# Optimization experiments

Measured on AMD Instinct MI355X. Metric: run time of the kernel, lower is better.

The kernel has to match this reference:

```python
import jax, jax.numpy as jnp
import numpy as np

S, L, E = 64, 256, 768          # sentences, tokens per sentence, BERT hidden
N, P = 4096, 32768              # events, event pairs
C, H, D = 256, 4, 64            # CGE channels, heads, head dim (C = H*D = n_last)
M = 8                           # max event span length
MLP_H = 1024
ITERS = 3                       # max_iteration + 1
RATE = 0.5
BETA_INTRA, BETA_INTER = 0.5, 0.5


def setup_inputs():
    key = jax.random.key(0)
    ks = jax.random.split(key, 16)
    nrm = lambda k, shape, sc: jax.random.normal(k, shape, dtype=jnp.float32) * sc
    event_start = jax.random.randint(ks[2], (N,), 0, L - M)
    span = jax.random.randint(ks[3], (N,), 1, M + 1)
    return {
        "sent_emb": nrm(ks[0], (S, L, E), 1.0),
        "proj_in_W": nrm(ks[7], (E, C), E ** -0.5),
        "proj_in_b": jnp.zeros((C,), jnp.float32),
        "proj_W": nrm(ks[8], (C, C), C ** -0.5),
        "proj_b": jnp.zeros((C,), jnp.float32),
        "att_src_intra": nrm(ks[9], (H, D), D ** -0.5),
        "att_dst_intra": nrm(ks[10], (H, D), D ** -0.5),
        "att_src_inter": nrm(ks[11], (H, D), D ** -0.5),
        "att_dst_inter": nrm(ks[12], (H, D), D ** -0.5),
        "mlp_W1": nrm(ks[13], (C + 2 * E, MLP_H), (C + 2 * E) ** -0.5),
        "mlp_b1": jnp.zeros((MLP_H,), jnp.float32),
        "mlp_W2": nrm(ks[14], (MLP_H, 3), MLP_H ** -0.5),
        "mlp_b2": jnp.zeros((3,), jnp.float32),
        "event_sent": jax.random.randint(ks[1], (N,), 0, S),
        "event_start": event_start,
        "event_end": event_start + span,
        "pair_idx": jax.random.randint(ks[4], (P, 2), 0, N),
        "rel_type": jax.random.randint(ks[5], (P,), 0, 2),
        "target": jax.random.randint(ks[6], (P,), 0, 3),
    }


def _attend(h, src, dst, emask, att_src, att_dst):
    # h: [N,H,D]. Masked graph attention, softmax over incoming edges per dst.
    a = jax.nn.leaky_relu((h[src] * att_src).sum(-1) + (h[dst] * att_dst).sum(-1), 0.2)  # [En,H]
    a = jnp.where(emask[:, None], a, -1e9)
    amax = jnp.maximum(jax.ops.segment_max(a, dst, num_segments=N), -1e9)  # [N,H]
    ex = jnp.exp(a - amax[dst]) * emask[:, None].astype(a.dtype)
    denom = jax.ops.segment_sum(ex, dst, num_segments=N)
    alpha = ex / (denom[dst] + 1e-9)
    out = jax.ops.segment_sum(alpha[:, :, None] * h[src], dst, num_segments=N)  # [N,H,D]
    return out.reshape(N, H * D)


def _forward(sent_emb, proj_in_W, proj_in_b, proj_W, proj_b,
             att_src_intra, att_dst_intra, att_src_inter, att_dst_inter,
             mlp_W1, mlp_b1, mlp_W2, mlp_b2,
             event_sent, event_start, event_end, pair_idx, rel_type, target):
    # extract_event: mean of sentence token embeddings over each event span
    pos = event_start[:, None] + jnp.arange(M)                      # [N,M]
    vmask = (pos < event_end[:, None]).astype(sent_emb.dtype)       # [N,M]
    tok = sent_emb[event_sent[:, None], jnp.clip(pos, 0, L - 1)]    # [N,M,E]
    e_emb = (tok * vmask[..., None]).sum(1) / (event_end - event_start).astype(sent_emb.dtype)[:, None]

    p0, p1 = pair_idx[:, 0], pair_idx[:, 1]
    pair_emb = jnp.concatenate([e_emb[p0], e_emb[p1]], axis=-1)     # [P,2E]
    x = e_emb @ proj_in_W + proj_in_b                               # [N,C]

    self_idx = jnp.arange(N)
    ones_n = jnp.ones((N,), bool)
    src_all = jnp.concatenate([p0, p1])
    dst_all = jnp.concatenate([p1, p0])
    intra2 = jnp.concatenate([rel_type == 0, rel_type == 0])

    loss = jnp.float32(0.0)
    pred = None
    for it in range(ITERS):
        diff = x[p0] - x[p1]                                        # [P,C]
        pre = jnp.concatenate([pair_emb, diff], axis=-1)            # [P,2E+C]
        pred = jax.nn.relu(pre @ mlp_W1 + mlp_b1) @ mlp_W2 + mlp_b2  # [P,3]
        logp = jax.nn.log_softmax(pred, axis=-1)
        loss = loss + (1.0 / (it + 1)) * (-jnp.take_along_axis(logp, target[:, None], axis=1).mean())

        # data-dependent edge construction (masked, fixed-size edge lists)
        psoft = jax.nn.softmax(pred, axis=-1)
        conf = psoft.max(1) > RATE
        parg = psoft.argmax(1)
        m_all = jnp.concatenate([conf & (parg == 1), conf & (parg == 2)])

        h = (x @ proj_W + proj_b).reshape(N, H, D)
        # intra edges + always-on self loops
        src_i = jnp.concatenate([src_all, self_idx])
        dst_i = jnp.concatenate([dst_all, self_idx])
        m_i = jnp.concatenate([m_all & intra2, ones_n])
        out_intra = _attend(h, src_i, dst_i, m_i, att_src_intra, att_dst_intra)
        out_inter = _attend(h, src_all, dst_all, m_all & (~intra2), att_src_inter, att_dst_inter)
        x = BETA_INTRA * out_intra + BETA_INTER * out_inter
    return loss, pred


def reference(sent_emb, proj_in_W, proj_in_b, proj_W, proj_b,
              att_src_intra, att_dst_intra, att_src_inter, att_dst_inter,
              mlp_W1, mlp_b1, mlp_W2, mlp_b2,
              event_sent, event_start, event_end, pair_idx, rel_type, target):
    return _forward(sent_emb, proj_in_W, proj_in_b, proj_W, proj_b,
                    att_src_intra, att_dst_intra, att_src_inter, att_dst_inter,
                    mlp_W1, mlp_b1, mlp_W2, mlp_b2,
                    event_sent, event_start, event_end, pair_idx, rel_type, target)
```

## Files before the change

### kernel.cpp

```cpp
#include <hip/hip_runtime.h>
#include <cstddef>
#include <cstdint>

#define NEV   4096
#define NPAIR 32768
#define NEDGE (2*NPAIR)
#define EDIM  768
#define CDIM  256
#define MLPH  1024
#define LLEN  256

typedef unsigned short u16;
typedef __attribute__((ext_vector_type(8))) short bhalf8;
typedef __attribute__((ext_vector_type(4))) float f32x4;

#define GLOAD_LDS(g, l) __builtin_amdgcn_global_load_lds( \
    (const __attribute__((address_space(1))) unsigned int*)(g), \
    (__attribute__((address_space(3))) unsigned int*)(l), 16, 0, 0)

__device__ inline u16 f2bf(float f) {
  union { float f; unsigned u; } v; v.f = f;
  unsigned r = v.u + 0x7fffu + ((v.u >> 16) & 1u);
  return (u16)(r >> 16);
}
__device__ inline float bf2f(u16 h) {
  union { unsigned u; float f; } v; v.u = ((unsigned)h) << 16; return v.f;
}

__global__ void k_zero(int* __restrict__ deg, int* __restrict__ pdeg,
                       float* __restrict__ out) {
  int i = blockIdx.x * 256 + threadIdx.x;
  if (i < NEV) { deg[i] = 0; pdeg[i] = 0; }
  if (i == 0) out[0] = 0.f;
}

__global__ void k_embed(const float* __restrict__ sent, const int* __restrict__ es,
                        const int* __restrict__ st, const int* __restrict__ en,
                        u16* __restrict__ Ahat) {
  int node = blockIdx.x;
  int s = es[node];
  int a = st[node];
  int span = en[node] - a;
  float fspan = (float)span;
  const float* base = sent + ((size_t)s * LLEN + a) * EDIM;
  for (int d = threadIdx.x; d < EDIM; d += 256) {
    float acc = 0.f;
    for (int m = 0; m < span; ++m) acc += base[(size_t)m * EDIM + d];
    float e = acc / fspan;
    u16 hi = f2bf(e);
    float lo = e - bf2f(hi);
    size_t b = (size_t)node * (2 * EDIM);
    Ahat[b + d] = hi;
    Ahat[b + EDIM + d] = f2bf(lo);
  }
}

__global__ void k_countF(const int* __restrict__ pair, int* __restrict__ deg,
                         int* __restrict__ pdeg) {
  int e = blockIdx.x * 256 + threadIdx.x;
  if (e >= NEDGE) return;
  int p = (e < NPAIR) ? e : e - NPAIR;
  int dst = (e < NPAIR) ? pair[2 * p + 1] : pair[2 * p];
  atomicAdd(&deg[dst], 1);
  if (e < NPAIR) atomicAdd(&pdeg[pair[2 * e]], 1);
}

__device__ inline void scan_body(const int* __restrict__ deg, int* __restrict__ rowp,
                                 int* __restrict__ cursor, int* part) {
  int t = threadIdx.x;
  int base = t * 16;
  int sum = 0;
  for (int i = 0; i < 16; ++i) sum += deg[base + i];
  part[t] = sum;
  __syncthreads();
  for (int off = 1; off < 256; off <<= 1) {
    int v = (t >= off) ? part[t - off] : 0;
    __syncthreads();
    part[t] += v;
    __syncthreads();
  }
  int run = (t == 0) ? 0 : part[t - 1];
  for (int i = 0; i < 16; ++i) {
    rowp[base + i] = run;
    cursor[base + i] = 0;
    run += deg[base + i];
  }
  if (t == 255) rowp[NEV] = run;
}

__global__ void k_scanF(const int* __restrict__ deg, int* __restrict__ rowp,
                        int* __restrict__ cursor, const int* __restrict__ pdeg,
                        int* __restrict__ prow, int* __restrict__ pcur) {
  __shared__ int part[256];
  scan_body(deg, rowp, cursor, part);
  __syncthreads();
  scan_body(pdeg, prow, pcur, part);
}

__global__ void k_scatterF(const int* __restrict__ pair, const int* __restrict__ rowp,
                           int* __restrict__ cursor, int* __restrict__ e_src,
                           int* __restrict__ e_id, const int* __restrict__ prow,
                           int* __restrict__ pcur, int* __restrict__ pidx) {
  int e = blockIdx.x * 256 + threadIdx.x;
  if (e >= NEDGE) return;
  int p   = (e < NPAIR) ? e : e - NPAIR;
  int src = (e < NPAIR) ? pair[2 * p]     : pair[2 * p + 1];
  int dst = (e < NPAIR) ? pair[2 * p + 1] : pair[2 * p];
  int pos = rowp[dst] + atomicAdd(&cursor[dst], 1);
  e_src[pos] = src;
  e_id[pos]  = e;
  if (e < NPAIR) {
    int pp = prow[pair[2 * e]] + atomicAdd(&pcur[pair[2 * e]], 1);
    pidx[pp] = e;
  }
}

__global__ __launch_bounds__(256) void cvt_w(const float* __restrict__ W1,
                                             const float* __restrict__ piW,
                                             const float* __restrict__ projW,
                                             u16* __restrict__ BTe,
                                             u16* __restrict__ BTu)
{
  __shared__ float tile[32][33];
  int which = (blockIdx.y >= 24) ? 1 : 0;
  if (which && blockIdx.x >= 40) return;
  u16* BT = which ? BTu : BTe;
  int K = which ? CDIM : EDIM;
  int ld = K * 2;
  int bk = (which ? (blockIdx.y - 24) : blockIdx.y) * 32;
  int bc = blockIdx.x * 32;
  int tx = threadIdx.x & 31, ty = threadIdx.x >> 5;
#pragma unroll
  for (int rr = 0; rr < 4; ++rr) {
    int k = bk + ty + rr * 8;
    int c = bc + tx;
    float v;
    if (which == 0) {
      v = (c < 1024) ? W1[(size_t)k * MLPH + c]
        : (c < 2048) ? W1[(size_t)(EDIM + k) * MLPH + (c - 1024)]
        : piW[(size_t)k * CDIM + (c - 2048)];
    } else {
      v = (c < 1024) ? W1[(size_t)(2 * EDIM + k) * MLPH + c]
        : projW[(size_t)k * CDIM + (c - 1024)];
    }
    tile[ty + rr * 8][tx] = v;
  }
  __syncthreads();
#pragma unroll
  for (int rr = 0; rr < 4; ++rr) {
    int c = bc + ty + rr * 8;
    int k = bk + tx;
    float v = tile[tx][ty + rr * 8];
    u16 hi = f2bf(v);
    float lo = v - bf2f(hi);
    size_t b = (size_t)c * ld;
    BT[b + k] = hi;
    BT[b + K + k] = f2bf(lo);
  }
}

__global__ __launch_bounds__(256) void mgemm(
    const u16* __restrict__ A, const u16* __restrict__ BT, int K, int mode,
    float* __restrict__ G1, float* __restrict__ G2, u16* __restrict__ Xhat,
    const float* __restrict__ pib, const float* __restrict__ b1,
    const float* __restrict__ pb, float* __restrict__ U, float* __restrict__ V,
    float* __restrict__ h, const float* __restrict__ asi,
    const float* __restrict__ adi, const float* __restrict__ asj,
    const float* __restrict__ adj, float* __restrict__ sv)
{
  __shared__ u16 Ash[64 * 32];
  __shared__ u16 Asl[64 * 32];
  __shared__ u16 Bsh[128 * 32];
  __shared__ u16 Bsl[128 * 32];
  int tid = threadIdx.x;
  int wave = tid >> 6, lane = tid & 63;
  int bm = blockIdx.y * 64, bn = blockIdx.x * 128;
  int wm = (wave >> 1) * 32, wn = (wave & 1) * 64;

  int Kp2 = 2 * K;
  int srow = tid >> 2;
  int scol = (tid & 3) << 3;
  const u16* AgH = A + (size_t)(bm + srow) * Kp2 + scol;
  const u16* BgH = BT + (size_t)(bn + srow) * Kp2 + scol;
  const u16* BgH2 = BT + (size_t)(bn + 64 + srow) * Kp2 + scol;

  f32x4 acc[2][4];
#pragma unroll
  for (int i = 0; i < 2; ++i)
#pragma unroll
    for (int j = 0; j < 4; ++j) {
      f32x4 z = {0.f, 0.f, 0.f, 0.f};
      acc[i][j] = z;
    }

  int fr = lane & 15;
  int fq = lane >> 4;

  for (int kc = 0; kc < K; kc += 32) {
    GLOAD_LDS(AgH + kc,       &Ash[tid * 8]);
    GLOAD_LDS(AgH + K + kc,   &Asl[tid * 8]);
    GLOAD_LDS(BgH + kc,       &Bsh[tid * 8]);
    GLOAD_LDS(BgH2 + kc,      &Bsh[2048 + tid * 8]);
    GLOAD_LDS(BgH + K + kc,   &Bsl[tid * 8]);
    GLOAD_LDS(BgH2 + K + kc,  &Bsl[2048 + tid * 8]);
    __syncthreads();
    bhalf8 afh[2], afl[2], bfh[4], bfl[4];
#pragma unroll
    for (int i = 0; i < 2; ++i) {
      afh[i] = *(const bhalf8*)&Ash[(wm + i * 16 + fr) * 32 + fq * 8];
      afl[i] = *(const bhalf8*)&Asl[(wm + i * 16 + fr) * 32 + fq * 8];
    }
#pragma unroll
    for (int j = 0; j < 4; ++j) {
      bfh[j] = *(const bhalf8*)&Bsh[(wn + j * 16 + fr) * 32 + fq * 8];
      bfl[j] = *(const bhalf8*)&Bsl[(wn + j * 16 + fr) * 32 + fq * 8];
    }
#pragma unroll
    for (int i = 0; i < 2; ++i)
#pragma unroll
      for (int j = 0; j < 4; ++j) {
        acc[i][j] = __builtin_amdgcn_mfma_f32_16x16x32_bf16(afh[i], bfh[j], acc[i][j], 0, 0, 0);
        acc[i][j] = __builtin_amdgcn_mfma_f32_16x16x32_bf16(afh[i], bfl[j], acc[i][j], 0, 0, 0);
        acc[i][j] = __builtin_amdgcn_mfma_f32_16x16x32_bf16(afl[i], bfh[j], acc[i][j], 0, 0, 0);
      }
    __syncthreads();
  }

#pragma unroll
  for (int i = 0; i < 2; ++i) {
    int mrow = bm + wm + i * 16 + fq * 4;
#pragma unroll
    for (int g = 0; g < 4; ++g) {
      int m = mrow + g;
#pragma unroll
      for (int j = 0; j < 4; ++j) {
        int c = bn + wn + j * 16 + fr;
        float vv = acc[i][j][g];
        if (mode == 0) {
          if (c < 1024) {
            G1[(size_t)m * MLPH + c] = vv;
          } else if (c < 2048) {
            G2[(size_t)m * MLPH + (c - 1024)] = vv;
          } else {
            int cc = c - 2048;
            float xv = vv + pib[cc];
            u16 hi = f2bf(xv);
            float lo = xv - bf2f(hi);
            size_t b = (size_t)m * (2 * CDIM);
            Xhat[b + cc] = hi;
            Xhat[b + CDIM + cc] = f2bf(lo);
          }
        } else {
          if (c < 1024) {
            size_t idx = (size_t)m * MLPH + c;
            U[idx] = G1[idx] + vv + b1[c];
            V[idx] = G2[idx] - vv;
          } else {
            int cc = c - 1024;
            h[(size_t)m * CDIM + cc] = vv + pb[cc];
          }
        }
      }
    }
  }

  if (mode == 1 && bn >= MLPH) {
    int hbase = bn - MLPH + wn;
    int head = hbase >> 6;
#pragma unroll
    for (int i = 0; i < 2; ++i) {
#pragma unroll
      for (int g = 0; g < 4; ++g) {
        int m = bm + wm + i * 16 + fq * 4 + g;
        float p0 = 0.f, p1 = 0.f, p2 = 0.f, p3 = 0.f;
#pragma unroll
        for (int j = 0; j < 4; ++j) {
          int hc = hbase + j * 16 + fr;
          float hv = acc[i][j][g] + pb[hc];
          p0 += hv * asi[hc];
          p1 += hv * adi[hc];
          p2 += hv * asj[hc];
          p3 += hv * adj[hc];
        }
#pragma unroll
        for (int mm = 1; mm < 16; mm <<= 1) {
          p0 += __shfl_xor(p0, mm);
          p1 += __shfl_xor(p1, mm);
          p2 += __shfl_xor(p2, mm);
          p3 += __shfl_xor(p3, mm);
        }
        if (fr == 0) {
          sv[0 * NEV * 4 + m * 4 + head] = p0;
          sv[1 * NEV * 4 + m * 4 + head] = p1;
          sv[2 * NEV * 4 + m * 4 + head] = p2;
          sv[3 * NEV * 4 + m * 4 + head] = p3;
        }
      }
    }
  }
}

__global__ __launch_bounds__(256) void k_pred_g(
    const float* __restrict__ U, const float* __restrict__ V,
    const int* __restrict__ pair, const int* __restrict__ prow,
    const int* __restrict__ pidx, const float* __restrict__ W2,
    const float* __restrict__ b2, const int* __restrict__ target,
    int* __restrict__ mstate, float* __restrict__ out,
    float* __restrict__ partials, float lossCoef)
{
  __shared__ float ush[MLPH];
  __shared__ float red[4];
  int n = blockIdx.x;
  int tid = threadIdx.x;
  const float* u = U + (size_t)n * MLPH;
#pragma unroll
  for (int i = 0; i < 4; ++i) ush[tid + i * 256] = u[tid + i * 256];
  __syncthreads();
  int wv = tid >> 6, lane = tid & 63;
  int beg = prow[n], end = prow[n + 1];
  float lsum = 0.f;
  for (int ip = beg + wv; ip < end; ip += 4) {
    int p = pidx[ip];
    int i1 = pair[2 * p + 1];
    const float* v = V + (size_t)i1 * MLPH;
    float a0 = 0.f, a1 = 0.f, a2 = 0.f;
    for (int kb = (lane << 2); kb < MLPH; kb += 256) {
      float4 uu = *(const float4*)(&ush[kb]);
      float4 vv = *(const float4*)(v + kb);
      float h0 = fmaxf(uu.x + vv.x, 0.f);
      float h1 = fmaxf(uu.y + vv.y, 0.f);
      float h2 = fmaxf(uu.z + vv.z, 0.f);
      float h3 = fmaxf(uu.w + vv.w, 0.f);
      const float4* w4 = (const float4*)(W2 + 3 * kb);
      float4 wa = w4[0], wb = w4[1], wc = w4[2];
      a0 += h0 * wa.x + h1 * wa.w + h2 * wb.z + h3 * wc.y;
      a1 += h0 * wa.y + h1 * wb.x + h2 * wb.w + h3 * wc.z;
      a2 += h0 * wa.z + h1 * wb.y + h2 * wc.x + h3 * wc.w;
    }
#pragma unroll
    for (int m = 32; m >= 1; m >>= 1) {
      a0 += __shfl_down(a0, m);
      a1 += __shfl_down(a1, m);
      a2 += __shfl_down(a2, m);
    }
    if (lane == 0) {
      a0 += b2[0]; a1 += b2[1]; a2 += b2[2];
      float mx = fmaxf(a0, fmaxf(a1, a2));
      float e0 = expf(a0 - mx), e1 = expf(a1 - mx), e2 = expf(a2 - mx);
      float sum = e0 + e1 + e2;
      int arg = 0; float best = e0;
      if (e1 > best) { best = e1; arg = 1; }
      if (e2 > best) { best = e2; arg = 2; }
      bool conf = (best / sum) > 0.5f;
      mstate[p] = conf ? arg : -1;
      int t = target[p];
      float predt = (t == 0) ? a0 : ((t == 1) ? a1 : a2);
      float logp = (predt - mx) - logf(sum);
      lsum += -logp * lossCoef;
      float* po = out + 1 + (size_t)p * 3;
      po[0] = a0; po[1] = a1; po[2] = a2;
    }
  }
  if (lane == 0) red[wv] = lsum;
  __syncthreads();
  if (tid == 0) partials[n] = red[0] + red[1] + red[2] + red[3];
}

__global__ __launch_bounds__(256) void k_attn(
    const float* __restrict__ h, const float* __restrict__ sv,
    const int* __restrict__ rowp, const int* __restrict__ e_src,
    const int* __restrict__ e_id, const int* __restrict__ mstate,
    const int* __restrict__ rel, u16* __restrict__ Xhat,
    const float* __restrict__ lpart, float* __restrict__ out)
{
  int node = blockIdx.x;
  int t = threadIdx.x;
  int head = t >> 6;
  const float* s_si = sv;
  const float* s_di = sv + NEV * 4;
  const float* s_sj = sv + 2 * NEV * 4;
  const float* s_dj = sv + 3 * NEV * 4;
  float sdi = s_di[node * 4 + head];
  float sdj = s_dj[node * 4 + head];
  int beg = rowp[node], end = rowp[node + 1];
  float aself = s_si[node * 4 + head] + sdi;
  aself = aself > 0.f ? aself : 0.2f * aself;
  float mxi = aself;
  float mxj = -1e9f;
  for (int e = beg; e < end; ++e) {
    int eid = e_id[e];
    int pp = (eid < NPAIR) ? eid : eid - NPAIR;
    int st = mstate[pp];
    bool mall = (eid < NPAIR) ? (st == 1) : (st == 2);
    if (!mall) continue;
    int src = e_src[e];
    if (rel[pp] == 0) {
      float a = s_si[src * 4 + head] + sdi;
      a = a > 0.f ? a : 0.2f * a;
      mxi = fmaxf(mxi, a);
    } else {
      float a = s_sj[src * 4 + head] + sdj;
      a = a > 0.f ? a : 0.2f * a;
      mxj = fmaxf(mxj, a);
    }
  }
  float deni = 0.f, denj = 0.f, acci = 0.f, accj = 0.f;
  {
    float ex = expf(aself - mxi);
    deni += ex;
    acci += ex * h[(size_t)node * CDIM + t];
  }
  for (int e = beg; e < end; ++e) {
    int eid = e_id[e];
    int pp = (eid < NPAIR) ? eid : eid - NPAIR;
    int st = mstate[pp];
    bool mall = (eid < NPAIR) ? (st == 1) : (st == 2);
    if (!mall) continue;
    int src = e_src[e];
    float hval = h[(size_t)src * CDIM + t];
    if (rel[pp] == 0) {
      float a = s_si[src * 4 + head] + sdi;
      a = a > 0.f ? a : 0.2f * a;
      float ex = expf(a - mxi);
      deni += ex; acci += ex * hval;
    } else {
      float a = s_sj[src * 4 + head] + sdj;
      a = a > 0.f ? a : 0.2f * a;
      float ex = expf(a - mxj);
      denj += ex; accj += ex * hval;
    }
  }
  float outv = 0.5f * (acci / (deni + 1e-9f)) + 0.5f * (accj / (denj + 1e-9f));
  u16 hi = f2bf(outv);
  float lo = outv - bf2f(hi);
  size_t b = (size_t)node * (2 * CDIM);
  Xhat[b + t] = hi;
  Xhat[b + CDIM + t] = f2bf(lo);

  if (blockIdx.x == 0) {
    __shared__ float sm[256];
    float s = 0.f;
    for (int i = t; i < NEV; i += 256) s += lpart[i];
    sm[t] = s;
    __syncthreads();
    for (int off = 128; off; off >>= 1) {
      if (t < off) sm[t] += sm[t + off];
      __syncthreads();
    }
    if (t == 0) out[0] += sm[0];
  }
}

extern "C" void kernel_launch(void* const* d_in, const int* in_sizes, int n_in,
                              void* d_out, int out_size, void* d_ws, size_t ws_size,
                              hipStream_t stream)
{
  const float* sent      = (const float*)d_in[0];
  const float* proj_in_W = (const float*)d_in[1];
  const float* proj_in_b = (const float*)d_in[2];
  const float* proj_W    = (const float*)d_in[3];
  const float* proj_b    = (const float*)d_in[4];
  const float* asi       = (const float*)d_in[5];
  const float* adi       = (const float*)d_in[6];
  const float* asj       = (const float*)d_in[7];
  const float* adj       = (const float*)d_in[8];
  const float* W1        = (const float*)d_in[9];
  const float* b1        = (const float*)d_in[10];
  const float* W2        = (const float*)d_in[11];
  const float* b2        = (const float*)d_in[12];
  const int*   es        = (const int*)d_in[13];
  const int*   st        = (const int*)d_in[14];
  const int*   en        = (const int*)d_in[15];
  const int*   pair      = (const int*)d_in[16];
  const int*   rel       = (const int*)d_in[17];
  const int*   target    = (const int*)d_in[18];
  float* out = (float*)d_out;

  char* w = (char*)d_ws;
  auto alloc = [&](size_t bytes) -> char* {
    char* p = w;
    w += (bytes + 255) & ~(size_t)255;
    return p;
  };
  u16*   Ahat = (u16*)alloc(sizeof(u16) * (size_t)NEV * 2 * EDIM);
  u16*   BTe  = (u16*)alloc(sizeof(u16) * (size_t)2304 * 1536);
  u16*   BTu  = (u16*)alloc(sizeof(u16) * (size_t)1280 * 512);
  u16*   Xhat = (u16*)alloc(sizeof(u16) * (size_t)NEV * 2 * CDIM);
  float* G1   = (float*)alloc(sizeof(float) * (size_t)NEV * MLPH);
  float* G2   = (float*)alloc(sizeof(float) * (size_t)NEV * MLPH);
  float* U    = (float*)alloc(sizeof(float) * (size_t)NEV * MLPH);
  float* V    = (float*)alloc(sizeof(float) * (size_t)NEV * MLPH);
  float* h    = (float*)alloc(sizeof(float) * (size_t)NEV * CDIM);
  float* sv   = (float*)alloc(sizeof(float) * (size_t)NEV * 16);
  float* lpart= (float*)alloc(sizeof(float) * NEV);
  int* deg    = (int*)alloc(sizeof(int) * NEV);
  int* rowp   = (int*)alloc(sizeof(int) * (NEV + 1));
  int* cursor = (int*)alloc(sizeof(int) * NEV);
  int* e_src  = (int*)alloc(sizeof(int) * NEDGE);
  int* e_id   = (int*)alloc(sizeof(int) * NEDGE);
  int* pdeg   = (int*)alloc(sizeof(int) * NEV);
  int* prow   = (int*)alloc(sizeof(int) * (NEV + 1));
  int* pcur   = (int*)alloc(sizeof(int) * NEV);
  int* pidx   = (int*)alloc(sizeof(int) * NPAIR);
  int* mstate = (int*)alloc(sizeof(int) * NPAIR);

  k_zero<<<(NEV + 255) / 256, 256, 0, stream>>>(deg, pdeg, out);
  k_embed<<<NEV, 256, 0, stream>>>(sent, es, st, en, Ahat);
  k_countF<<<NEDGE / 256, 256, 0, stream>>>(pair, deg, pdeg);
  k_scanF<<<1, 256, 0, stream>>>(deg, rowp, cursor, pdeg, prow, pcur);
  k_scatterF<<<NEDGE / 256, 256, 0, stream>>>(pair, rowp, cursor, e_src, e_id,
                                              prow, pcur, pidx);
  cvt_w<<<dim3(72, 32), 256, 0, stream>>>(W1, proj_in_W, proj_W, BTe, BTu);

  mgemm<<<dim3(2304 / 128, NEV / 64), 256, 0, stream>>>(
      Ahat, BTe, EDIM, 0, G1, G2, Xhat, proj_in_b,
      nullptr, nullptr, nullptr, nullptr, nullptr,
      nullptr, nullptr, nullptr, nullptr, nullptr);

  for (int it = 0; it < 3; ++it) {
    mgemm<<<dim3(1280 / 128, NEV / 64), 256, 0, stream>>>(
        Xhat, BTu, CDIM, 1, G1, G2, nullptr, nullptr,
        b1, proj_b, U, V, h, asi, adi, asj, adj, sv);
    float coef = 1.0f / ((float)(it + 1) * (float)NPAIR);
    k_pred_g<<<NEV, 256, 0, stream>>>(U, V, pair, prow, pidx, W2, b2, target,
                                      mstate, out, lpart, coef);
    k_attn<<<NEV, 256, 0, stream>>>(h, sv, rowp, e_src, e_id, mstate, rel, Xhat,
                                    lpart, out);
  }
  (void)in_sizes; (void)n_in; (void)out_size; (void)ws_size;
}
```

Before: 503.8 us.

## Double-buffer GEMM LDS staging and merge prep kernels into one launch

```diff
diff --git a/kernel.cpp b/kernel.cpp
--- a/kernel.cpp
+++ b/kernel.cpp
@@ -27,32 +27,86 @@
   union { unsigned u; float f; } v; v.u = ((unsigned)h) << 16; return v.f;
 }
 
-__global__ void k_zero(int* __restrict__ deg, int* __restrict__ pdeg,
-                       float* __restrict__ out) {
-  int i = blockIdx.x * 256 + threadIdx.x;
+__global__ __launch_bounds__(256) void k_prep(
+    const float* __restrict__ sent, const int* __restrict__ es,
+    const int* __restrict__ st, const int* __restrict__ en,
+    u16* __restrict__ Ahat, const float* __restrict__ W1,
+    const float* __restrict__ piW, const float* __restrict__ projW,
+    u16* __restrict__ BTe, u16* __restrict__ BTu,
+    int* __restrict__ deg, int* __restrict__ pdeg, float* __restrict__ out)
+{
+  __shared__ float tile[32][33];
+  int b = blockIdx.x;
+  int tid = threadIdx.x;
+  if (b < NEV) {
+    int node = b;
+    int s = es[node];
+    int a = st[node];
+    int span = en[node] - a;
+    float fspan = (float)span;
+    const float* base = sent + ((size_t)s * LLEN + a) * EDIM;
+    if (tid < 192) {
+      int d0 = tid * 4;
+      float4 acc = {0.f, 0.f, 0.f, 0.f};
+      for (int m = 0; m < span; ++m) {
+        float4 v = *(const float4*)(base + (size_t)m * EDIM + d0);
+        acc.x += v.x; acc.y += v.y; acc.z += v.z; acc.w += v.w;
+      }
+      float e[4] = {acc.x / fspan, acc.y / fspan, acc.z / fspan, acc.w / fspan};
+      ushort4 hiv, lov;
+      u16 h0 = f2bf(e[0]); lov.x = f2bf(e[0] - bf2f(h0)); hiv.x = h0;
+      u16 h1 = f2bf(e[1]); lov.y = f2bf(e[1] - bf2f(h1)); hiv.y = h1;
+      u16 h2 = f2bf(e[2]); lov.z = f2bf(e[2] - bf2f(h2)); hiv.z = h2;
+      u16 h3 = f2bf(e[3]); lov.w = f2bf(e[3] - bf2f(h3)); hiv.w = h3;
+      size_t bo = (size_t)node * (2 * EDIM);
+      *(ushort4*)&Ahat[bo + d0] = hiv;
+      *(ushort4*)&Ahat[bo + EDIM + d0] = lov;
+    }
+    return;
+  }
+  if (b < NEV + 2304) {
+    int id = b - NEV;
+    int bxx = id % 72, byy = id / 72;
+    int which = (byy >= 24) ? 1 : 0;
+    if (which && bxx >= 40) return;
+    u16* BT = which ? BTu : BTe;
+    int K = which ? CDIM : EDIM;
+    int ld = K * 2;
+    int bk = (which ? (byy - 24) : byy) * 32;
+    int bc = bxx * 32;
+    int tx = tid & 31, ty = tid >> 5;
+#pragma unroll
+    for (int rr = 0; rr < 4; ++rr) {
+      int k = bk + ty + rr * 8;
+      int c = bc + tx;
+      float v;
+      if (which == 0) {
+        v = (c < 1024) ? W1[(size_t)k * MLPH + c]
+          : (c < 2048) ? W1[(size_t)(EDIM + k) * MLPH + (c - 1024)]
+          : piW[(size_t)k * CDIM + (c - 2048)];
+      } else {
+        v = (c < 1024) ? W1[(size_t)(2 * EDIM + k) * MLPH + c]
+          : projW[(size_t)k * CDIM + (c - 1024)];
+      }
+      tile[ty + rr * 8][tx] = v;
+    }
+    __syncthreads();
+#pragma unroll
+    for (int rr = 0; rr < 4; ++rr) {
+      int c = bc + ty + rr * 8;
+      int k = bk + tx;
+      float v = tile[tx][ty + rr * 8];
+      u16 hi = f2bf(v);
+      float lo = v - bf2f(hi);
+      size_t bb = (size_t)c * ld;
+      BT[bb + k] = hi;
+      BT[bb + K + k] = f2bf(lo);
+    }
+    return;
+  }
+  int i = (b - NEV - 2304) * 256 + tid;
   if (i < NEV) { deg[i] = 0; pdeg[i] = 0; }
   if (i == 0) out[0] = 0.f;
-}
-
-__global__ void k_embed(const float* __restrict__ sent, const int* __restrict__ es,
-                        const int* __restrict__ st, const int* __restrict__ en,
-                        u16* __restrict__ Ahat) {
-  int node = blockIdx.x;
-  int s = es[node];
-  int a = st[node];
-  int span = en[node] - a;
-  float fspan = (float)span;
-  const float* base = sent + ((size_t)s * LLEN + a) * EDIM;
-  for (int d = threadIdx.x; d < EDIM; d += 256) {
-    float acc = 0.f;
-    for (int m = 0; m < span; ++m) acc += base[(size_t)m * EDIM + d];
-    float e = acc / fspan;
-    u16 hi = f2bf(e);
-    float lo = e - bf2f(hi);
-    size_t b = (size_t)node * (2 * EDIM);
-    Ahat[b + d] = hi;
-    Ahat[b + EDIM + d] = f2bf(lo);
-  }
 }
 
 __global__ void k_countF(const int* __restrict__ pair, int* __restrict__ deg,
@@ -115,50 +169,6 @@
   }
 }
 
-__global__ __launch_bounds__(256) void cvt_w(const float* __restrict__ W1,
-                                             const float* __restrict__ piW,
-                                             const float* __restrict__ projW,
-                                             u16* __restrict__ BTe,
-                                             u16* __restrict__ BTu)
-{
-  __shared__ float tile[32][33];
-  int which = (blockIdx.y >= 24) ? 1 : 0;
-  if (which && blockIdx.x >= 40) return;
-  u16* BT = which ? BTu : BTe;
-  int K = which ? CDIM : EDIM;
-  int ld = K * 2;
-  int bk = (which ? (blockIdx.y - 24) : blockIdx.y) * 32;
-  int bc = blockIdx.x * 32;
-  int tx = threadIdx.x & 31, ty = threadIdx.x >> 5;
-#pragma unroll
-  for (int rr = 0; rr < 4; ++rr) {
-    int k = bk + ty + rr * 8;
-    int c = bc + tx;
-    float v;
-    if (which == 0) {
-      v = (c < 1024) ? W1[(size_t)k * MLPH + c]
-        : (c < 2048) ? W1[(size_t)(EDIM + k) * MLPH + (c - 1024)]
-        : piW[(size_t)k * CDIM + (c - 2048)];
-    } else {
-      v = (c < 1024) ? W1[(size_t)(2 * EDIM + k) * MLPH + c]
-        : projW[(size_t)k * CDIM + (c - 1024)];
-    }
-    tile[ty + rr * 8][tx] = v;
-  }
-  __syncthreads();
-#pragma unroll
-  for (int rr = 0; rr < 4; ++rr) {
-    int c = bc + ty + rr * 8;
-    int k = bk + tx;
-    float v = tile[tx][ty + rr * 8];
-    u16 hi = f2bf(v);
-    float lo = v - bf2f(hi);
-    size_t b = (size_t)c * ld;
-    BT[b + k] = hi;
-    BT[b + K + k] = f2bf(lo);
-  }
-}
-
 __global__ __launch_bounds__(256) void mgemm(
     const u16* __restrict__ A, const u16* __restrict__ BT, int K, int mode,
     float* __restrict__ G1, float* __restrict__ G2, u16* __restrict__ Xhat,
@@ -168,10 +178,10 @@
     const float* __restrict__ adi, const float* __restrict__ asj,
     const float* __restrict__ adj, float* __restrict__ sv)
 {
-  __shared__ u16 Ash[64 * 32];
-  __shared__ u16 Asl[64 * 32];
-  __shared__ u16 Bsh[128 * 32];
-  __shared__ u16 Bsl[128 * 32];
+  __shared__ u16 Ash[2 * 64 * 32];
+  __shared__ u16 Asl[2 * 64 * 32];
+  __shared__ u16 Bsh[2 * 128 * 32];
+  __shared__ u16 Bsl[2 * 128 * 32];
   int tid = threadIdx.x;
   int wave = tid >> 6, lane = tid & 63;
   int bm = blockIdx.y * 64, bn = blockIdx.x * 128;
@@ -180,9 +190,22 @@
   int Kp2 = 2 * K;
   int srow = tid >> 2;
   int scol = (tid & 3) << 3;
-  const u16* AgH = A + (size_t)(bm + srow) * Kp2 + scol;
-  const u16* BgH = BT + (size_t)(bn + srow) * Kp2 + scol;
+  const u16* AgH  = A + (size_t)(bm + srow) * Kp2 + scol;
+  const u16* BgH  = BT + (size_t)(bn + srow) * Kp2 + scol;
   const u16* BgH2 = BT + (size_t)(bn + 64 + srow) * Kp2 + scol;
+
+  auto STAGE = [&](int buf, int kc) {
+    u16* as = Ash + buf * 2048;
+    u16* al = Asl + buf * 2048;
+    u16* bs = Bsh + buf * 4096;
+    u16* bl = Bsl + buf * 4096;
+    GLOAD_LDS(AgH + kc,       &as[tid * 8]);
+    GLOAD_LDS(AgH + K + kc,   &al[tid * 8]);
+    GLOAD_LDS(BgH + kc,       &bs[tid * 8]);
+    GLOAD_LDS(BgH2 + kc,      &bs[2048 + tid * 8]);
+    GLOAD_LDS(BgH + K + kc,   &bl[tid * 8]);
+    GLOAD_LDS(BgH2 + K + kc,  &bl[2048 + tid * 8]);
+  };
 
   f32x4 acc[2][4];
 #pragma unroll
@@ -196,24 +219,25 @@
   int fr = lane & 15;
   int fq = lane >> 4;
 
+  STAGE(0, 0);
+  __syncthreads();
+  int cur = 0;
   for (int kc = 0; kc < K; kc += 32) {
-    GLOAD_LDS(AgH + kc,       &Ash[tid * 8]);
-    GLOAD_LDS(AgH + K + kc,   &Asl[tid * 8]);
-    GLOAD_LDS(BgH + kc,       &Bsh[tid * 8]);
-    GLOAD_LDS(BgH2 + kc,      &Bsh[2048 + tid * 8]);
-    GLOAD_LDS(BgH + K + kc,   &Bsl[tid * 8]);
-    GLOAD_LDS(BgH2 + K + kc,  &Bsl[2048 + tid * 8]);
-    __syncthreads();
+    if (kc + 32 < K) STAGE(cur ^ 1, kc + 32);
+    const u16* as = Ash + cur * 2048;
+    const u16* al = Asl + cur * 2048;
+    const u16* bs = Bsh + cur * 4096;
+    const u16* bl = Bsl + cur * 4096;
     bhalf8 afh[2], afl[2], bfh[4], bfl[4];
 #pragma unroll
     for (int i = 0; i < 2; ++i) {
-      afh[i] = *(const bhalf8*)&Ash[(wm + i * 16 + fr) * 32 + fq * 8];
-      afl[i] = *(const bhalf8*)&Asl[(wm + i * 16 + fr) * 32 + fq * 8];
+      afh[i] = *(const bhalf8*)&as[(wm + i * 16 + fr) * 32 + fq * 8];
+      afl[i] = *(const bhalf8*)&al[(wm + i * 16 + fr) * 32 + fq * 8];
     }
 #pragma unroll
     for (int j = 0; j < 4; ++j) {
-      bfh[j] = *(const bhalf8*)&Bsh[(wn + j * 16 + fr) * 32 + fq * 8];
-      bfl[j] = *(const bhalf8*)&Bsl[(wn + j * 16 + fr) * 32 + fq * 8];
+      bfh[j] = *(const bhalf8*)&bs[(wn + j * 16 + fr) * 32 + fq * 8];
+      bfl[j] = *(const bhalf8*)&bl[(wn + j * 16 + fr) * 32 + fq * 8];
     }
 #pragma unroll
     for (int i = 0; i < 2; ++i)
@@ -224,6 +248,7 @@
         acc[i][j] = __builtin_amdgcn_mfma_f32_16x16x32_bf16(afl[i], bfh[j], acc[i][j], 0, 0, 0);
       }
     __syncthreads();
+    cur ^= 1;
   }
 
 #pragma unroll
@@ -504,13 +529,13 @@
   int* pidx   = (int*)alloc(sizeof(int) * NPAIR);
   int* mstate = (int*)alloc(sizeof(int) * NPAIR);
 
-  k_zero<<<(NEV + 255) / 256, 256, 0, stream>>>(deg, pdeg, out);
-  k_embed<<<NEV, 256, 0, stream>>>(sent, es, st, en, Ahat);
+  k_prep<<<NEV + 2304 + 16, 256, 0, stream>>>(sent, es, st, en, Ahat,
+                                              W1, proj_in_W, proj_W, BTe, BTu,
+                                              deg, pdeg, out);
   k_countF<<<NEDGE / 256, 256, 0, stream>>>(pair, deg, pdeg);
   k_scanF<<<1, 256, 0, stream>>>(deg, rowp, cursor, pdeg, prow, pcur);
   k_scatterF<<<NEDGE / 256, 256, 0, stream>>>(pair, rowp, cursor, e_src, e_id,
                                               prow, pcur, pidx);
-  cvt_w<<<dim3(72, 32), 256, 0, stream>>>(W1, proj_in_W, proj_W, BTe, BTu);
 
   mgemm<<<dim3(2304 / 128, NEV / 64), 256, 0, stream>>>(
       Ahat, BTe, EDIM, 0, G1, G2, Xhat, proj_in_b,
```

After: 484.0 us. 1.04x faster.
